# Kernel optimization log

Hardware: AMD Instinct MI355X
Metric: run time of the kernel (lower is better)

## Reference

```python
import jax, jax.numpy as jnp
import numpy as np

B, N, D = 4, 256, 128


def setup_inputs() -> dict:
    key = jax.random.key(0)
    kx, kw = jax.random.split(key)
    x = jax.random.normal(kx, (B, N, D), dtype=jnp.float32)
    # xavier_uniform with gain=calculate_gain('relu')=sqrt(2)
    bound = float(np.sqrt(2.0) * np.sqrt(6.0 / (D + D)))
    W = jax.random.uniform(kw, (D, D), minval=-bound, maxval=bound, dtype=jnp.float32)
    return {"x": x, "W": W}


def _normalize(adj):
    # preprocess(): A_norm = D^{-1/2} A D^{-1/2} with D = diag(row-sums)
    deg = jnp.sum(adj, axis=2)                      # [B, N]
    dinv = jax.lax.rsqrt(deg)                       # deg^{-0.5}
    return dinv[:, :, None] * adj * dinv[:, None, :]


def reference(x, W):
    Bn, Nn, _ = x.shape
    eye = jnp.broadcast_to(jnp.eye(Nn, dtype=x.dtype), (Bn, Nn, Nn))
    # initial step: adj = I, so conv(x, I) = x @ W
    x = jax.nn.relu(x @ W)
    idx = jnp.arange(Nn)

    def step(carry, i):
        x, adj, adj_out = carry
        x_i = x[:, i, :]                            # x_last, [B, D]
        prob = jnp.einsum('bnd,bd->bn', x, x_i)     # x_prev . x_last for all nodes
        mask = idx < i                              # keep only cols/rows 0:i

        def upd(A):
            A = A.at[:, i, :].set(jnp.where(mask, prob, A[:, i, :]))
            A = A.at[:, :, i].set(jnp.where(mask, prob, A[:, :, i]))
            return A

        adj_out = upd(adj_out)
        adj = upd(adj)                              # mutate previously-normalized adj (matches torch)
        adj_n = _normalize(adj)
        y = jnp.einsum('bij,bjd->bid', adj_n, x)    # adj @ x
        x = jax.nn.relu(y @ W)                      # GraphConv + ReLU
        return (x, adj_n, adj_out), None

    (x, adj, adj_out), _ = jax.lax.scan(step, (x, eye, eye), jnp.arange(1, Nn))
    return adj_out
```

## Files before the change

kernel.cpp:

```cpp
#include <hip/hip_runtime.h>
#include <hip/hip_cooperative_groups.h>

namespace cg = cooperative_groups;

#define NB 4
#define NN 256
#define ND 128

#define LDS_FLOATS 21896

__device__ __forceinline__ float2 ld2(const float* p) {
    return *reinterpret_cast<const float2*>(p);
}

__device__ __forceinline__ float2 ldc2(const float* p) {
    unsigned long long u = __hip_atomic_load((unsigned long long*)p,
                              __ATOMIC_RELAXED, __HIP_MEMORY_SCOPE_AGENT);
    union { unsigned long long u; float2 f; } c; c.u = u; return c.f;
}
__device__ __forceinline__ void stc2(float* p, float2 v) {
    union { unsigned long long u; float2 f; } c; c.f = v;
    __hip_atomic_store((unsigned long long*)p, c.u,
                       __ATOMIC_RELAXED, __HIP_MEMORY_SCOPE_AGENT);
}
__device__ __forceinline__ float ldc(const float* p) {
    unsigned u = __hip_atomic_load((unsigned*)p,
                    __ATOMIC_RELAXED, __HIP_MEMORY_SCOPE_AGENT);
    return __uint_as_float(u);
}
__device__ __forceinline__ void stc(float* p, float v) {
    __hip_atomic_store((unsigned*)p, __float_as_uint(v),
                       __ATOMIC_RELAXED, __HIP_MEMORY_SCOPE_AGENT);
}

__device__ __forceinline__ void batch_barrier(int* flg, int step, int w) {
    __syncthreads();
    if (threadIdx.x == 0)
        __hip_atomic_store(flg + w, step, __ATOMIC_RELAXED, __HIP_MEMORY_SCOPE_AGENT);
    if (threadIdx.x < 64) {
        while (__hip_atomic_load(flg + threadIdx.x, __ATOMIC_RELAXED,
                                 __HIP_MEMORY_SCOPE_AGENT) < step)
            __builtin_amdgcn_s_sleep(1);
    }
    asm volatile("" ::: "memory");
    __syncthreads();
}

extern "C" __global__ void __launch_bounds__(256, 1)
gcn_coop_kernel(const float* __restrict__ Xin, const float* __restrict__ Wg,
                float* __restrict__ out, float* __restrict__ ws)
{
    extern __shared__ float lds[];
    float* Wl    = lds;
    float* Al    = lds + 16384;
    float* xi    = lds + 17408;
    float* prob  = lds + 17536;
    float* dinv  = lds + 17792;
    float* arow  = lds + 18048;
    float* srow  = lds + 18304;
    float* ypart = lds + 19328;
    float* yrow  = lds + 21376;
    float* red   = lds + 21888;

    const int tid  = threadIdx.x;
    const int lane = tid & 63;
    const int v    = tid >> 6;
    const int b    = (blockIdx.x & 7) >> 1;
    const int w    = (blockIdx.x & 1) * 32 + (blockIdx.x >> 3);
    const int n0   = w << 2;
    const int nv   = n0 + v;

    float* X0  = ws;
    float* X1  = X0 + NB*NN*ND;
    float* R0  = X1 + NB*NN*ND;
    float* R1  = R0 + NB*NN;
    float* AR0 = R1 + NB*NN;
    float* AR1 = AR0 + NB*NN;
    int*   flg = (int*)(AR1 + NB*NN);

    {
        const float4* Wg4 = reinterpret_cast<const float4*>(Wg);
        float4* Wl4 = reinterpret_cast<float4*>(Wl);
        #pragma unroll
        for (int k = 0; k < 16; ++k) Wl4[tid + 256*k] = Wg4[tid + 256*k];
    }
    {
        const float2* src = reinterpret_cast<const float2*>(Xin + (b*NN + nv)*ND);
        reinterpret_cast<float2*>(yrow + v*ND)[lane] = src[lane];
    }
    if (tid == 0)
        __hip_atomic_store(flg + b*64 + w, 0, __ATOMIC_RELAXED, __HIP_MEMORY_SCOPE_AGENT);
    __syncthreads();

    {
        float a0 = 0.f, a1 = 0.f;
        const float4* yr4 = reinterpret_cast<const float4*>(yrow + v*ND);
        #pragma unroll 4
        for (int dd = 0; dd < 32; ++dd) {
            float4 y4 = yr4[dd];
            float2 w0 = ld2(Wl + (4*dd+0)*ND + 2*lane);
            float2 w1 = ld2(Wl + (4*dd+1)*ND + 2*lane);
            float2 w2 = ld2(Wl + (4*dd+2)*ND + 2*lane);
            float2 w3 = ld2(Wl + (4*dd+3)*ND + 2*lane);
            a0 += y4.x*w0.x; a1 += y4.x*w0.y;
            a0 += y4.y*w1.x; a1 += y4.y*w1.y;
            a0 += y4.z*w2.x; a1 += y4.z*w2.y;
            a0 += y4.w*w3.x; a1 += y4.w*w3.y;
        }
        float2 r; r.x = fmaxf(a0, 0.f); r.y = fmaxf(a1, 0.f);
        stc2(X0 + (b*NN+nv)*ND + 2*lane, r);
        #pragma unroll
        for (int rr = 0; rr < 4; ++rr)
            Al[rr*NN + tid] = (tid == n0 + rr) ? 1.f : 0.f;
        if (lane == 0) {
            stc(R0 + b*NN + nv, 1.f);
            out[(b*NN+nv)*NN + nv] = 1.f;
        }
        if (w == 0) stc(AR0 + b*NN + tid, (tid == 1) ? 1.f : 0.f);
    }

    cg::grid_group grid = cg::this_grid();

    for (int i = 1; i < NN; ++i) {
        if (i == 1) grid.sync();
        else        batch_barrier(flg + b*64, i, w);
        const int cur = (i-1) & 1;
        const float* Xc  = cur ? X1 : X0;
        float*       Xn  = cur ? X0 : X1;
        const float* Rc  = cur ? R1 : R0;
        float*       Rn  = cur ? R0 : R1;
        const float* ARc = cur ? AR1 : AR0;
        float*       ARn = cur ? AR0 : AR1;

        if (tid < 64) {
            float2 t = ldc2(Xc + (b*NN+i)*ND + 2*tid);
            reinterpret_cast<float2*>(xi)[tid] = t;
        }
        arow[tid] = ldc(ARc + b*NN + tid);
        __syncthreads();

        float pv = 0.f;
        if (tid < i) {
            const float* xr = Xc + (b*NN+tid)*ND;
            float p0 = 0.f, p1 = 0.f;
            #pragma unroll 16
            for (int k = 0; k < 64; ++k) {
                float2 a = ldc2(xr + 2*k);
                p0 += a.x * xi[2*k];
                p1 += a.y * xi[2*k+1];
            }
            pv = p0 + p1;
        }
        float pd = (tid < i) ? (pv - arow[tid]) : 0.f;
        #pragma unroll
        for (int off = 32; off; off >>= 1) pd += __shfl_down(pd, off, 64);
        if (lane == 0) red[v] = pd;
        prob[tid] = pv;
        __syncthreads();

        {
            const float rc = ldc(Rc + b*NN + tid);
            float deg;
            if (tid < i)      deg = rc - arow[tid] + pv;
            else if (tid > i) deg = rc;
            else              deg = rc + red[0] + red[1] + red[2] + red[3];
            dinv[tid] = rsqrtf(deg);
        }
        __syncthreads();

        {
            const int j = tid;
            const float dj = dinv[j];
            float sv[4];
            #pragma unroll
            for (int r = 0; r < 4; ++r) {
                const int n = n0 + r;
                float m;
                if (n == i)      m = (j < i) ? prob[j] : Al[r*NN + j];
                else if (j == i) m = (n < i) ? prob[n] : Al[r*NN + j];
                else             m = Al[r*NN + j];
                const float s = m * dj;
                sv[r] = s;
                Al[r*NN + j] = dinv[n] * s;
                if (n == i && j < i) out[(b*NN+i)*NN + j] = prob[j];
            }
            if (j == i) {
                #pragma unroll
                for (int r = 0; r < 4; ++r) {
                    const int n = n0 + r;
                    if (n < i) out[(b*NN+n)*NN + i] = prob[n];
                }
            }
            reinterpret_cast<float4*>(srow)[j] = make_float4(sv[0], sv[1], sv[2], sv[3]);
        }
        __syncthreads();

        if (i < NN-1) {
            {
                const unsigned rr = (unsigned)(i + 1 - n0);
                if (rr < 4u) stc(ARn + b*NN + tid, Al[rr*NN + tid]);
            }
            {
                float sacc = srow[lane*4 + v] + srow[(lane+64)*4 + v]
                           + srow[(lane+128)*4 + v] + srow[(lane+192)*4 + v];
                #pragma unroll
                for (int off = 32; off; off >>= 1) sacc += __shfl_down(sacc, off, 64);
                if (lane == 0) stc(Rn + b*NN + nv, dinv[nv] * sacc);
            }
            float y0x=0,y0y=0,y1x=0,y1y=0,y2x=0,y2y=0,y3x=0,y3y=0;
            const float* XcB    = Xc + b*NN*ND;
            const float4* srow4 = reinterpret_cast<const float4*>(srow);
            #pragma unroll 8
            for (int jj = 0; jj < 64; ++jj) {
                const int jB = v*64 + jj;
                const float4 s  = srow4[jB];
                const float2 xv = ldc2(XcB + jB*ND + 2*lane);
                y0x += s.x*xv.x; y0y += s.x*xv.y;
                y1x += s.y*xv.x; y1y += s.y*xv.y;
                y2x += s.z*xv.x; y2y += s.z*xv.y;
                y3x += s.w*xv.x; y3y += s.w*xv.y;
            }
            float2* yp2 = reinterpret_cast<float2*>(ypart);
            yp2[(v*4+0)*64 + lane] = make_float2(y0x,y0y);
            yp2[(v*4+1)*64 + lane] = make_float2(y1x,y1y);
            yp2[(v*4+2)*64 + lane] = make_float2(y2x,y2y);
            yp2[(v*4+3)*64 + lane] = make_float2(y3x,y3y);
            __syncthreads();
            {
                float2 a  = yp2[(0*4+v)*64 + lane];
                float2 t1 = yp2[(1*4+v)*64 + lane];
                float2 t2 = yp2[(2*4+v)*64 + lane];
                float2 t3 = yp2[(3*4+v)*64 + lane];
                a.x += t1.x + t2.x + t3.x;
                a.y += t1.y + t2.y + t3.y;
                const float dn = dinv[nv];
                a.x *= dn; a.y *= dn;
                reinterpret_cast<float2*>(yrow + v*ND)[lane] = a;
            }
            {
                float a0 = 0.f, a1 = 0.f;
                const float4* yr4 = reinterpret_cast<const float4*>(yrow + v*ND);
                #pragma unroll 4
                for (int dd = 0; dd < 32; ++dd) {
                    float4 y4 = yr4[dd];
                    float2 w0 = ld2(Wl + (4*dd+0)*ND + 2*lane);
                    float2 w1 = ld2(Wl + (4*dd+1)*ND + 2*lane);
                    float2 w2 = ld2(Wl + (4*dd+2)*ND + 2*lane);
                    float2 w3 = ld2(Wl + (4*dd+3)*ND + 2*lane);
                    a0 += y4.x*w0.x; a1 += y4.x*w0.y;
                    a0 += y4.y*w1.x; a1 += y4.y*w1.y;
                    a0 += y4.z*w2.x; a1 += y4.z*w2.y;
                    a0 += y4.w*w3.x; a1 += y4.w*w3.y;
                }
                float2 r; r.x = fmaxf(a0, 0.f); r.y = fmaxf(a1, 0.f);
                stc2(Xn + (b*NN+nv)*ND + 2*lane, r);
            }
        }
    }
}

extern "C" void kernel_launch(void* const* d_in, const int* in_sizes, int n_in,
                              void* d_out, int out_size, void* d_ws, size_t ws_size,
                              hipStream_t stream)
{
    const float* x  = (const float*)d_in[0];
    const float* W  = (const float*)d_in[1];
    float* out      = (float*)d_out;
    float* ws       = (float*)d_ws;
    (void)in_sizes; (void)n_in; (void)out_size; (void)ws_size;

    hipFuncSetAttribute(reinterpret_cast<const void*>(gcn_coop_kernel),
                        hipFuncAttributeMaxDynamicSharedMemorySize,
                        LDS_FLOATS * 4);

    void* args[] = { (void*)&x, (void*)&W, (void*)&out, (void*)&ws };
    hipLaunchCooperativeKernel(reinterpret_cast<void*>(gcn_coop_kernel),
                               dim3(NB*64), dim3(256),
                               args, LDS_FLOATS * 4, stream);
}
```

Before: 4.288 ms.

## Store node features as bf16 and stage full batch X tile in LDS

Node features exchanged between blocks each step are now packed to bf16 in the workspace, which halves global traffic. Each block copies its batch's whole X matrix into LDS once per step, using a padded stride, and both the similarity dot products and the adj@x product read from LDS instead of issuing scattered atomic global loads. This cuts per-step global latency and bandwidth, but every block now loads all 256 rows each step and LDS use grows. Features are rounded to bf16, which changes numerics in the recurrent adjacency computation and may compound over 255 steps.

```diff
diff --git a/kernel.cpp b/kernel.cpp
--- a/kernel.cpp
+++ b/kernel.cpp
@@ -7,30 +7,36 @@
 #define NN 256
 #define ND 128
 
-#define LDS_FLOATS 21896
+#define LDS_FLOATS 38408
 
 __device__ __forceinline__ float2 ld2(const float* p) {
     return *reinterpret_cast<const float2*>(p);
 }
 
-__device__ __forceinline__ float2 ldc2(const float* p) {
-    unsigned long long u = __hip_atomic_load((unsigned long long*)p,
-                              __ATOMIC_RELAXED, __HIP_MEMORY_SCOPE_AGENT);
-    union { unsigned long long u; float2 f; } c; c.u = u; return c.f;
-}
-__device__ __forceinline__ void stc2(float* p, float2 v) {
-    union { unsigned long long u; float2 f; } c; c.f = v;
-    __hip_atomic_store((unsigned long long*)p, c.u,
-                       __ATOMIC_RELAXED, __HIP_MEMORY_SCOPE_AGENT);
+__device__ __forceinline__ unsigned long long ldcu8(const unsigned long long* p) {
+    return __hip_atomic_load(p, __ATOMIC_RELAXED, __HIP_MEMORY_SCOPE_AGENT);
 }
 __device__ __forceinline__ float ldc(const float* p) {
-    unsigned u = __hip_atomic_load((unsigned*)p,
+    unsigned u = __hip_atomic_load((const unsigned*)p,
                     __ATOMIC_RELAXED, __HIP_MEMORY_SCOPE_AGENT);
     return __uint_as_float(u);
 }
 __device__ __forceinline__ void stc(float* p, float v) {
     __hip_atomic_store((unsigned*)p, __float_as_uint(v),
                        __ATOMIC_RELAXED, __HIP_MEMORY_SCOPE_AGENT);
+}
+__device__ __forceinline__ void stcu(unsigned* p, unsigned v) {
+    __hip_atomic_store(p, v, __ATOMIC_RELAXED, __HIP_MEMORY_SCOPE_AGENT);
+}
+
+__device__ __forceinline__ unsigned f2bf(float f) {
+    unsigned u = __float_as_uint(f);
+    return (u + 0x7fffu + ((u >> 16) & 1u)) >> 16;
+}
+__device__ __forceinline__ float bflo(unsigned w) { return __uint_as_float(w << 16); }
+__device__ __forceinline__ float bfhi(unsigned w) { return __uint_as_float(w & 0xffff0000u); }
+__device__ __forceinline__ unsigned packbf(float a, float b) {
+    return f2bf(a) | (f2bf(b) << 16);
 }
 
 __device__ __forceinline__ void batch_barrier(int* flg, int step, int w) {
@@ -51,16 +57,16 @@
                 float* __restrict__ out, float* __restrict__ ws)
 {
     extern __shared__ float lds[];
-    float* Wl    = lds;
-    float* Al    = lds + 16384;
-    float* xi    = lds + 17408;
-    float* prob  = lds + 17536;
-    float* dinv  = lds + 17792;
-    float* arow  = lds + 18048;
-    float* srow  = lds + 18304;
-    float* ypart = lds + 19328;
-    float* yrow  = lds + 21376;
-    float* red   = lds + 21888;
+    float*    Wl    = lds;
+    unsigned* Xlu   = (unsigned*)(lds + 16384);
+    float*    Al    = lds + 33024;
+    float*    prob  = lds + 34048;
+    float*    dinv  = lds + 34304;
+    float*    arow  = lds + 34560;
+    float*    srow  = lds + 34816;
+    float*    ypart = lds + 35840;
+    float*    yrow  = lds + 37888;
+    float*    red   = lds + 38400;
 
     const int tid  = threadIdx.x;
     const int lane = tid & 63;
@@ -70,13 +76,13 @@
     const int n0   = w << 2;
     const int nv   = n0 + v;
 
-    float* X0  = ws;
-    float* X1  = X0 + NB*NN*ND;
-    float* R0  = X1 + NB*NN*ND;
-    float* R1  = R0 + NB*NN;
-    float* AR0 = R1 + NB*NN;
-    float* AR1 = AR0 + NB*NN;
-    int*   flg = (int*)(AR1 + NB*NN);
+    unsigned* XU0 = (unsigned*)ws;
+    unsigned* XU1 = XU0 + NB*NN*64;
+    float*    R0  = (float*)(XU1 + NB*NN*64);
+    float*    R1  = R0 + NB*NN;
+    float*    AR0 = R1 + NB*NN;
+    float*    AR1 = AR0 + NB*NN;
+    int*      flg = (int*)(AR1 + NB*NN);
 
     {
         const float4* Wg4 = reinterpret_cast<const float4*>(Wg);
@@ -107,8 +113,7 @@
             a0 += y4.z*w2.x; a1 += y4.z*w2.y;
             a0 += y4.w*w3.x; a1 += y4.w*w3.y;
         }
-        float2 r; r.x = fmaxf(a0, 0.f); r.y = fmaxf(a1, 0.f);
-        stc2(X0 + (b*NN+nv)*ND + 2*lane, r);
+        stcu(XU0 + (b*NN+nv)*64 + lane, packbf(fmaxf(a0,0.f), fmaxf(a1,0.f)));
         #pragma unroll
         for (int rr = 0; rr < 4; ++rr)
             Al[rr*NN + tid] = (tid == n0 + rr) ? 1.f : 0.f;
@@ -125,29 +130,40 @@
         if (i == 1) grid.sync();
         else        batch_barrier(flg + b*64, i, w);
         const int cur = (i-1) & 1;
-        const float* Xc  = cur ? X1 : X0;
-        float*       Xn  = cur ? X0 : X1;
+        const unsigned* Xcu = cur ? XU1 : XU0;
+        unsigned*       Xnu = cur ? XU0 : XU1;
         const float* Rc  = cur ? R1 : R0;
         float*       Rn  = cur ? R0 : R1;
         const float* ARc = cur ? AR1 : AR0;
         float*       ARn = cur ? AR0 : AR1;
 
-        if (tid < 64) {
-            float2 t = ldc2(Xc + (b*NN+i)*ND + 2*tid);
-            reinterpret_cast<float2*>(xi)[tid] = t;
+        {
+            const unsigned long long* src =
+                reinterpret_cast<const unsigned long long*>(Xcu + b*NN*64);
+            #pragma unroll
+            for (int k = 0; k < 32; ++k) {
+                const int q   = tid + (k << 8);
+                unsigned long long d = ldcu8(src + q);
+                const int row = q >> 5;
+                const int c2  = (q & 31) << 1;
+                Xlu[row*65 + c2]     = (unsigned)d;
+                Xlu[row*65 + c2 + 1] = (unsigned)(d >> 32);
+            }
         }
         arow[tid] = ldc(ARc + b*NN + tid);
         __syncthreads();
 
         float pv = 0.f;
         if (tid < i) {
-            const float* xr = Xc + (b*NN+tid)*ND;
+            const unsigned* xr = Xlu + tid*65;
+            const unsigned* xc = Xlu + i*65;
             float p0 = 0.f, p1 = 0.f;
             #pragma unroll 16
             for (int k = 0; k < 64; ++k) {
-                float2 a = ldc2(xr + 2*k);
-                p0 += a.x * xi[2*k];
-                p1 += a.y * xi[2*k+1];
+                const unsigned a = xr[k];
+                const unsigned c = xc[k];
+                p0 += bflo(a) * bflo(c);
+                p1 += bfhi(a) * bfhi(c);
             }
             pv = p0 + p1;
         }
@@ -208,17 +224,17 @@
                 if (lane == 0) stc(Rn + b*NN + nv, dinv[nv] * sacc);
             }
             float y0x=0,y0y=0,y1x=0,y1y=0,y2x=0,y2y=0,y3x=0,y3y=0;
-            const float* XcB    = Xc + b*NN*ND;
             const float4* srow4 = reinterpret_cast<const float4*>(srow);
             #pragma unroll 8
             for (int jj = 0; jj < 64; ++jj) {
                 const int jB = v*64 + jj;
                 const float4 s  = srow4[jB];
-                const float2 xv = ldc2(XcB + jB*ND + 2*lane);
-                y0x += s.x*xv.x; y0y += s.x*xv.y;
-                y1x += s.y*xv.x; y1y += s.y*xv.y;
-                y2x += s.z*xv.x; y2y += s.z*xv.y;
-                y3x += s.w*xv.x; y3y += s.w*xv.y;
+                const unsigned xw = Xlu[jB*65 + lane];
+                const float xvx = bflo(xw), xvy = bfhi(xw);
+                y0x += s.x*xvx; y0y += s.x*xvy;
+                y1x += s.y*xvx; y1y += s.y*xvy;
+                y2x += s.z*xvx; y2y += s.z*xvy;
+                y3x += s.w*xvx; y3y += s.w*xvy;
             }
             float2* yp2 = reinterpret_cast<float2*>(ypart);
             yp2[(v*4+0)*64 + lane] = make_float2(y0x,y0y);
@@ -252,8 +268,7 @@
                     a0 += y4.z*w2.x; a1 += y4.z*w2.y;
                     a0 += y4.w*w3.x; a1 += y4.w*w3.y;
                 }
-                float2 r; r.x = fmaxf(a0, 0.f); r.y = fmaxf(a1, 0.f);
-                stc2(Xn + (b*NN+nv)*ND + 2*lane, r);
+                stcu(Xnu + (b*NN+nv)*64 + lane, packbf(fmaxf(a0,0.f), fmaxf(a1,0.f)));
             }
         }
     }
```

After: 4.518 ms. 5.4% more time.
